# Performance work log

Measured on AMD Instinct MI355X. Metric: run time of the kernel, lower is better.

## Reference

```python
import jax, jax.numpy as jnp
import numpy as np
import math

B, T, DIM = 2, 2048, 4096
N_HEADS, N_KV_HEADS = 32, 8
HEAD_DIM = DIM // N_HEADS          # 128
N_REP = N_HEADS // N_KV_HEADS      # 4
ROPE_THETA = 500000.0
NEG_INF = -1e9


def setup_inputs() -> dict:
    key = jax.random.key(0)
    ks = jax.random.split(key, 5)
    x = jax.random.normal(ks[0], (B, T, DIM), dtype=jnp.float32)
    # rotary angles: theta_j = pos * base^(-2j/d), shape [T, HEAD_DIM//2]
    inv_freq = 1.0 / (ROPE_THETA ** (jnp.arange(0, HEAD_DIM, 2, dtype=jnp.float32) / HEAD_DIM))
    freqs = jnp.arange(T, dtype=jnp.float32)[:, None] * inv_freq[None, :]
    # causal additive mask [T, T]
    mask = jnp.where(jnp.tril(jnp.ones((T, T), dtype=bool)), 0.0, NEG_INF).astype(jnp.float32)
    s = 0.02
    wq = jax.random.normal(ks[1], (DIM, N_HEADS * HEAD_DIM), dtype=jnp.float32) * s
    wk = jax.random.normal(ks[2], (DIM, N_KV_HEADS * HEAD_DIM), dtype=jnp.float32) * s
    wv = jax.random.normal(ks[3], (DIM, N_KV_HEADS * HEAD_DIM), dtype=jnp.float32) * s
    wo = jax.random.normal(ks[4], (N_HEADS * HEAD_DIM, DIM), dtype=jnp.float32) * s
    return {"x": x, "freqs": freqs, "mask": mask, "wq": wq, "wk": wk, "wv": wv, "wo": wo, "start_pos": 0}


def _apply_rope(x, cos, sin):
    # x: [B, T, H, D]; cos/sin: [T, D//2]; adjacent pairs rotated (view-as-complex)
    xr = x[..., 0::2]
    xi = x[..., 1::2]
    c = cos[None, :, None, :]
    s = sin[None, :, None, :]
    out_r = xr * c - xi * s
    out_i = xr * s + xi * c
    return jnp.stack([out_r, out_i], axis=-1).reshape(x.shape)


def reference(x, freqs, mask, wq, wk, wv, wo, start_pos):
    Bx, Tx, C = x.shape
    xq = (x @ wq).reshape(Bx, Tx, N_HEADS, HEAD_DIM)
    xk = (x @ wk).reshape(Bx, Tx, N_KV_HEADS, HEAD_DIM)
    xv = (x @ wv).reshape(Bx, Tx, N_KV_HEADS, HEAD_DIM)
    cos, sin = jnp.cos(freqs), jnp.sin(freqs)
    xq = _apply_rope(xq, cos, sin)
    xk = _apply_rope(xk, cos, sin)
    # repeat_kv for GQA: [B, T, Hkv, D] -> [B, T, Hkv*n_rep, D]
    xk = jnp.repeat(xk, N_REP, axis=2)
    xv = jnp.repeat(xv, N_REP, axis=2)
    q = xq.transpose(0, 2, 1, 3)  # [B, H, T, D]
    k = xk.transpose(0, 2, 1, 3)
    v = xv.transpose(0, 2, 1, 3)
    scores = jnp.einsum("bhtd,bhsd->bhts", q, k) / math.sqrt(HEAD_DIM)
    scores = scores + mask[None, None, :, :]
    probs = jax.nn.softmax(scores.astype(jnp.float32), axis=-1).astype(q.dtype)
    out = jnp.einsum("bhts,bhsd->bhtd", probs, v)
    out = out.transpose(0, 2, 1, 3).reshape(Bx, Tx, -1)
    return out @ wo
```

## Files before the change

kernel.cpp:

```cpp
#include <hip/hip_runtime.h>
#include <cstdint>
#include <cstddef>

typedef float  f32x4  __attribute__((ext_vector_type(4)));
typedef short  bf16x8 __attribute__((ext_vector_type(8)));
typedef unsigned short u16;
typedef u16    u16x8  __attribute__((ext_vector_type(8)));
typedef unsigned int u32;

#define T_SEQ 2048
#define N_HEADS 32
#define N_KVH 8
#define HD 128
#define QSCALE 0.12751743648963412f

__device__ __forceinline__ u16 f2bf(float f){
  union { float f; unsigned u; } v; v.f = f;
  unsigned u = v.u;
  u += 0x7fffu + ((u >> 16) & 1u);
  return (u16)(u >> 16);
}

__device__ __forceinline__ u32 cvt_pk_bf16(float a, float b){
  u32 r;
  asm volatile("v_cvt_pk_bf16_f32 %0, %1, %2" : "=v"(r) : "v"(a), "v"(b));
  return r;
}

__device__ __forceinline__ void gll16(const void* g, void* l){
  __builtin_amdgcn_global_load_lds((const __attribute__((address_space(1))) void*)g,
                                   (__attribute__((address_space(3))) void*)l, 16, 0, 0);
}

__device__ __forceinline__ u32 lds_addr(const void* p){
  return (u32)(size_t)(__attribute__((address_space(3))) const void*)p;
}

__global__ void mk_tables(const float* __restrict__ f, float* __restrict__ c, float* __restrict__ s,
                          float* __restrict__ ct, float* __restrict__ st){
  int i = blockIdx.x*256 + threadIdx.x;
  float v = f[i];
  float cv = cosf(v), sv = sinf(v);
  c[i] = cv;
  s[i] = sv;
  int t = i >> 6, d = i & 63;
  ct[d*T_SEQ + t] = cv;
  st[d*T_SEQ + t] = sv;
}

__global__ void cvt_bf16(const float* __restrict__ in, u16* __restrict__ out){
  size_t i = (size_t)blockIdx.x*256 + threadIdx.x;
  const float4* p = (const float4*)(in + i*8);
  float4 a = p[0], b = p[1];
  u16x8 o;
  o[0]=f2bf(a.x); o[1]=f2bf(a.y); o[2]=f2bf(a.z); o[3]=f2bf(a.w);
  o[4]=f2bf(b.x); o[5]=f2bf(b.y); o[6]=f2bf(b.z); o[7]=f2bf(b.w);
  *(u16x8*)(out + i*8) = o;
}

__global__ void wtrans(const float* __restrict__ W, u16* __restrict__ Wt, int K, int N){
  __shared__ float t[32][33];
  int tx = threadIdx.x, ty = threadIdx.y;
  int nb = blockIdx.x*32, kb = blockIdx.y*32;
#pragma unroll
  for (int j=0;j<4;j++) t[ty+8*j][tx] = W[(size_t)(kb+ty+8*j)*N + nb + tx];
  __syncthreads();
#pragma unroll
  for (int j=0;j<4;j++) Wt[(size_t)(nb+ty+8*j)*K + kb + tx] = f2bf(t[tx][ty+8*j]);
}

template<int BN>
__global__ __launch_bounds__(512, 2) void gemm256(
    const u16* __restrict__ A, const u16* __restrict__ Bt,
    float* __restrict__ C, int N, int K)
{
  constexpr int NGB = BN/64;
  constexpr int NF  = BN/64;
  __shared__ u16 Ab[2][16384];
  __shared__ u16 Bb[2][BN*64];
  const int tid = threadIdx.x;
  const int w = tid >> 6, lane = tid & 63;
  const int lo = lane & 15, hi = lane >> 4;

  const int nbx = N / BN;
  const int cpx = (int)gridDim.x >> 3;
  const int swzb = ((int)blockIdx.x & 7)*cpx + ((int)blockIdx.x >> 3);
  const int bx = swzb % nbx, by = swzb / nbx;
  const int m0 = by << 8, n0 = bx * BN;
  const int wm = w >> 2, wn = w & 3;

  const int rA = tid >> 3;
  const int chg = (tid & 7) ^ (rA & 7);
  const size_t srcoff = (size_t)rA * K + chg*8;
  const u16* Ag = A  + (size_t)m0*K + srcoff;
  const u16* Bg = Bt + (size_t)n0*K + srcoff;
  const int dstc = (w*64)*8;

  f32x4 acc[8][NF];
#pragma unroll
  for (int i=0;i<8;i++)
#pragma unroll
    for (int j=0;j<NF;j++) acc[i][j] = (f32x4){0.f,0.f,0.f,0.f};

  const int NT = K >> 6;
#pragma unroll
  for (int j=0;j<4;j++)   gll16(Ag + (size_t)j*64*K, &Ab[0][j*4096 + dstc]);
#pragma unroll
  for (int j=0;j<NGB;j++) gll16(Bg + (size_t)j*64*K, &Bb[0][j*4096 + dstc]);

  const int sw = lo & 7;
#pragma unroll 1
  for (int t=0; t<NT; ++t){
    const int cur = t & 1;
    if (t > 0){
      asm volatile("s_waitcnt lgkmcnt(0)" ::: "memory");
      __builtin_amdgcn_s_barrier();
    }
    if (t + 1 < NT){
      const int kt = (t+1) << 6;
      const int nxt = cur ^ 1;
#pragma unroll
      for (int j=0;j<4;j++)   gll16(Ag + (size_t)j*64*K + kt, &Ab[nxt][j*4096 + dstc]);
#pragma unroll
      for (int j=0;j<NGB;j++) gll16(Bg + (size_t)j*64*K + kt, &Bb[nxt][j*4096 + dstc]);
      if constexpr (BN == 256){
        asm volatile("s_waitcnt vmcnt(8)" ::: "memory");
      } else {
        asm volatile("s_waitcnt vmcnt(6)" ::: "memory");
      }
    } else {
      asm volatile("s_waitcnt vmcnt(0)" ::: "memory");
    }
    __builtin_amdgcn_s_barrier();
    __builtin_amdgcn_sched_barrier(0);

    const u16* Ac = &Ab[cur][0] + (wm*128)*64;
    const u16* Bc = &Bb[cur][0] + (wn*(BN/4))*64;
    bf16x8 a[4], b[NF];
#pragma unroll
    for (int ks=0; ks<2; ks++){
      const int ch = ((ks*4 + hi) ^ sw) << 3;
#pragma unroll
      for (int g=0; g<NF; g++) b[g] = *(const bf16x8*)(Bc + (g*16 + lo)*64 + ch);
#pragma unroll
      for (int mh=0; mh<2; mh++){
#pragma unroll
        for (int f=0; f<4; f++) a[f] = *(const bf16x8*)(Ac + (mh*64 + f*16 + lo)*64 + ch);
        __builtin_amdgcn_s_setprio(1);
#pragma unroll
        for (int f=0; f<4; f++)
#pragma unroll
          for (int g=0; g<NF; g++)
            acc[mh*4+f][g] = __builtin_amdgcn_mfma_f32_16x16x32_bf16(a[f], b[g], acc[mh*4+f][g], 0, 0, 0);
        __builtin_amdgcn_s_setprio(0);
      }
    }
  }

#pragma unroll
  for (int mh=0; mh<2; mh++)
#pragma unroll
    for (int f=0; f<4; f++)
#pragma unroll
      for (int g=0; g<NF; g++)
#pragma unroll
        for (int r=0; r<4; r++)
          C[(size_t)(m0 + wm*128 + mh*64 + f*16 + hi*4 + r)*N + n0 + wn*(BN/4) + g*16 + lo] = acc[mh*4+f][g][r];
}

#define RDA(BK, RGS, MH) { _Pragma("unroll") for (int f=0; f<4; f++) \
    asm volatile("ds_read_b128 %0, %1 offset:" RGS : "=v"(BK[f]) : "v"(aAddr[MH][f])); }
#define RDB(BK, RGS) { _Pragma("unroll") for (int g=0; g<4; g++) \
    asm volatile("ds_read_b128 %0, %1 offset:" RGS : "=v"(BK[g]) : "v"(bAddr[g])); }
#define STGA8(RG, KO) { gll16(Ag + offs0 + (KO), AL + (RG) + wofs); gll16(Ag + offs1 + (KO), AL + (RG) + 4096 + wofs); }
#define STGB8(RG, KO) { gll16(Bg + offs0 + (KO), BL + (RG) + wofs); gll16(Bg + offs1 + (KO), BL + (RG) + 4096 + wofs); }
#define MFMAB(AB, BB, MH) { _Pragma("unroll") for (int f=0; f<4; f++) _Pragma("unroll") for (int g=0; g<4; g++) \
    acc[(MH)*4+f][g] = __builtin_amdgcn_mfma_f32_16x16x32_bf16(AB[f], BB[g], acc[(MH)*4+f][g], 0, 0, 0); }
#define PH_HEAD() { __builtin_amdgcn_sched_barrier(0); __builtin_amdgcn_s_barrier(); \
    asm volatile("s_waitcnt lgkmcnt(0)" ::: "memory"); __builtin_amdgcn_sched_barrier(0); __builtin_amdgcn_s_setprio(1); }
#define PH_TAIL() { __builtin_amdgcn_s_setprio(0); __builtin_amdgcn_s_barrier(); }

__global__ __launch_bounds__(512, 2) void gemm8p(
    const u16* __restrict__ A, const u16* __restrict__ Bt,
    float* __restrict__ C, int N, int K)
{
  __shared__ u16 AL[32768];
  __shared__ u16 BL[32768];
  const int tid = threadIdx.x;
  const int w = tid >> 6, lane = tid & 63;
  const int lo = lane & 15, hi = lane >> 4;

  const int nbx = N >> 8;
  const int cpx = (int)gridDim.x >> 3;
  const int swzb = ((int)blockIdx.x & 7)*cpx + ((int)blockIdx.x >> 3);
  const int bx = swzb % nbx, by = swzb / nbx;
  const int m0 = by << 8, n0 = bx << 8;
  const int wm = w >> 2, wn = w & 3;

  u32 aAddr[2][4], bAddr[4];
#pragma unroll
  for (int mh=0; mh<2; mh++)
#pragma unroll
    for (int f=0; f<4; f++){
      int row = wm*128 + mh*64 + f*16 + lo;
      int p = row >> 1;
      aAddr[mh][f] = lds_addr(AL) + (u32)((p*8 + (((row&1)*4 + hi) ^ (p&7)))*16);
    }
#pragma unroll
  for (int g=0; g<4; g++){
    int row = wn*64 + g*16 + lo;
    int p = row >> 1;
    bAddr[g] = lds_addr(BL) + (u32)((p*8 + (((row&1)*4 + hi) ^ (p&7)))*16);
  }

  int offs0, offs1;
  {
    int n = tid;
    int p = n>>3, e = (n&7) ^ (p&7);
    offs0 = (p*2 + (e>>2))*K + (e&3)*8;
    n = 512 + tid;
    p = n>>3; e = (n&7) ^ (p&7);
    offs1 = (p*2 + (e>>2))*K + (e&3)*8;
  }
  const u16* Ag = A  + (size_t)m0*K;
  const u16* Bg = Bt + (size_t)n0*K;
  const int wofs = w*512;

  f32x4 acc[8][4];
#pragma unroll
  for (int i=0;i<8;i++)
#pragma unroll
    for (int j=0;j<4;j++) acc[i][j] = (f32x4){0.f,0.f,0.f,0.f};

  const int NT = K >> 6;
  bf16x8 aA[4], aB[4], bA[4], bB[4];

  STGA8(0, 0)       STGB8(0, 0)
  STGA8(8192, 32)   STGB8(8192, 32)
  STGA8(16384, 64)  STGB8(16384, 64)
  asm volatile("s_waitcnt vmcnt(8)" ::: "memory");
  __builtin_amdgcn_s_barrier();
  RDA(aA, "0", 0) RDB(bA, "0")

#pragma unroll 1
  for (int u = 0; u < NT-2; u += 2){
    const int ku = u*64;
    STGA8(24576, ku+96)
    PH_HEAD() RDA(aB, "0", 1) MFMAB(aA, bA, 0) PH_TAIL()
    STGB8(24576, ku+96)
    asm volatile("s_waitcnt vmcnt(8)" ::: "memory");
    PH_HEAD() RDA(aA, "16384", 0) RDB(bB, "16384") MFMAB(aB, bA, 1) PH_TAIL()
    STGA8(0, ku+128)
    PH_HEAD() RDA(aB, "16384", 1) MFMAB(aA, bB, 0) PH_TAIL()
    STGB8(0, ku+128)
    asm volatile("s_waitcnt vmcnt(8)" ::: "memory");
    PH_HEAD() RDA(aA, "32768", 0) RDB(bA, "32768") MFMAB(aB, bB, 1) PH_TAIL()
    STGA8(8192, ku+160)
    PH_HEAD() RDA(aB, "32768", 1) MFMAB(aA, bA, 0) PH_TAIL()
    STGB8(8192, ku+160)
    asm volatile("s_waitcnt vmcnt(8)" ::: "memory");
    PH_HEAD() RDA(aA, "49152", 0) RDB(bB, "49152") MFMAB(aB, bA, 1) PH_TAIL()
    STGA8(16384, ku+192)
    PH_HEAD() RDA(aB, "49152", 1) MFMAB(aA, bB, 0) PH_TAIL()
    STGB8(16384, ku+192)
    asm volatile("s_waitcnt vmcnt(8)" ::: "memory");
    PH_HEAD() RDA(aA, "0", 0) RDB(bA, "0") MFMAB(aB, bB, 1) PH_TAIL()
  }

  {
    const int ku = (NT-2)*64;
    STGA8(24576, ku+96)
    PH_HEAD() RDA(aB, "0", 1) MFMAB(aA, bA, 0) PH_TAIL()
    STGB8(24576, ku+96)
    asm volatile("s_waitcnt vmcnt(8)" ::: "memory");
    PH_HEAD() RDA(aA, "16384", 0) RDB(bB, "16384") MFMAB(aB, bA, 1) PH_TAIL()
    PH_HEAD() RDA(aB, "16384", 1) MFMAB(aA, bB, 0) PH_TAIL()
    asm volatile("s_waitcnt vmcnt(4)" ::: "memory");
    PH_HEAD() RDA(aA, "32768", 0) RDB(bA, "32768") MFMAB(aB, bB, 1) PH_TAIL()
    PH_HEAD() RDA(aB, "32768", 1) MFMAB(aA, bA, 0) PH_TAIL()
    asm volatile("s_waitcnt vmcnt(0)" ::: "memory");
    PH_HEAD() RDA(aA, "49152", 0) RDB(bB, "49152") MFMAB(aB, bA, 1) PH_TAIL()
    PH_HEAD() RDA(aB, "49152", 1) MFMAB(aA, bB, 0) PH_TAIL()
    PH_HEAD() MFMAB(aB, bB, 1) PH_TAIL()
  }

#pragma unroll
  for (int mh=0; mh<2; mh++)
#pragma unroll
    for (int f=0; f<4; f++)
#pragma unroll
      for (int g=0; g<4; g++)
#pragma unroll
        for (int r=0; r<4; r++)
          C[(size_t)(m0 + wm*128 + mh*64 + f*16 + hi*4 + r)*N + n0 + wn*64 + g*16 + lo] = acc[mh*4+f][g][r];
}

__global__ void rope_k(const float* __restrict__ kvf, const float* __restrict__ c,
                       const float* __restrict__ s, u16* __restrict__ kb){
  const int row = blockIdx.x;
  const int b = row >> 11, t = row & (T_SEQ-1);
  const float* ib = kvf + (size_t)row*2048;
#pragma unroll
  for (int k=0;k<2;k++){
    int p = threadIdx.x + k*256;
    int kvh = p >> 6, i = p & 63;
    float cv = c[t*64+i], sv = s[t*64+i];
    float2 v = *(const float2*)(ib + 2*p);
    float vr = v.x*cv - v.y*sv;
    float vi = v.x*sv + v.y*cv;
    u16* o = kb + ((size_t)(b*N_KVH+kvh)*T_SEQ + t)*HD + 2*i;
    ushort2 ov; ov.x = f2bf(vr); ov.y = f2bf(vi);
    *(ushort2*)o = ov;
  }
}

__global__ void vtrans(const float* __restrict__ kvf, u16* __restrict__ vt){
  __shared__ float tl[32][33];
  int tx = threadIdx.x, ty = threadIdx.y;
  int t0 = blockIdx.x*32, d0 = blockIdx.y*32, bh = blockIdx.z;
  int b = bh >> 3, kvh = bh & 7;
#pragma unroll
  for (int j=0;j<4;j++)
    tl[ty+8*j][tx] = kvf[(size_t)(b*T_SEQ + t0+ty+8*j)*2048 + 1024 + kvh*HD + d0 + tx];
  __syncthreads();
#pragma unroll
  for (int j=0;j<4;j++)
    vt[((size_t)bh*HD + d0+ty+8*j)*T_SEQ + t0 + tx] = f2bf(tl[tx][ty+8*j]);
}

#define KVB 64
__global__ __launch_bounds__(512) void attn_kernel(
    const float* __restrict__ qf, const float* __restrict__ costT, const float* __restrict__ sintT,
    const u16* __restrict__ kb, const u16* __restrict__ vt, u16* __restrict__ attn)
{
  __shared__ u16 KV[2][2][8192];

  const int tid = threadIdx.x;
  const int lane = tid & 63, wid = tid >> 6;
  const int lo = lane & 15, hi = lane >> 4;
  const bool lowhi = (hi < 2);
  const int bp0 = lo + 32*(hi & 1);
  const int bp1 = bp0 + 16;
  const int h = blockIdx.y, b = blockIdx.z;
  const int kvh = h >> 2;
  const int qt = b ? (int)blockIdx.x : 7 - (int)blockIdx.x;
  const int q0 = qt*256 + wid*32;
  const int ntiles = (qt+1)*4;

  int koff[2], voff[2];
#pragma unroll
  for (int p=0;p<2;p++){
    int s = p*512 + tid;
    int kr = s >> 4, kch = (s & 15) ^ (kr & 7);
    koff[p] = kr*HD + kch*8;
    int vd = s >> 3, vch = (s & 7) ^ (vd & 7);
    voff[p] = vd*T_SEQ + vch*8;
  }
  const u16* Kg = kb + (size_t)(b*N_KVH + kvh)*T_SEQ*HD;
  const u16* Vg = vt + (size_t)(b*N_KVH + kvh)*HD*T_SEQ;

  bf16x8 qfr[2][4];
#pragma unroll
  for (int mb=0;mb<2;mb++){
    const int t = q0 + mb*16 + lo;
    const float* qrow = qf + (size_t)(b*T_SEQ + t)*4096 + h*HD;
#pragma unroll
    for (int kc=0;kc<4;kc++){
      f32x4 v0 = *(const f32x4*)(qrow + kc*32 + hi*8);
      f32x4 v1 = *(const f32x4*)(qrow + kc*32 + hi*8 + 4);
      union { u32 w[4]; bf16x8 v; } pk;
#pragma unroll
      for (int j=0;j<4;j++){
        int i = kc*16 + hi*4 + j;
        float cv = costT[i*T_SEQ + t], sv = sintT[i*T_SEQ + t];
        float xr = (j<2) ? v0[2*j]   : v1[2*(j-2)];
        float xi = (j<2) ? v0[2*j+1] : v1[2*(j-2)+1];
        float vr = (xr*cv - xi*sv)*QSCALE;
        float vi = (xr*sv + xi*cv)*QSCALE;
        pk.w[j] = ((u32)f2bf(vi) << 16) | (u32)f2bf(vr);
      }
      qfr[mb][kc] = pk.v;
    }
  }

  f32x4 acc[2][8];
#pragma unroll
  for (int mb=0;mb<2;mb++)
#pragma unroll
    for (int nd=0;nd<8;nd++) acc[mb][nd] = (f32x4){0.f,0.f,0.f,0.f};
  float m_[2] = {-3.0e38f, -3.0e38f};
  float l_[2] = {0.f, 0.f};

#pragma unroll
  for (int p=0;p<2;p++){
    gll16(Kg + koff[p], (u16*)&KV[0][0][0] + (p*512 + wid*64)*8);
    gll16(Vg + voff[p], (u16*)&KV[0][1][0] + (p*512 + wid*64)*8);
  }

#pragma unroll 1
  for (int st=0; st<ntiles; ++st){
    const int cur = st & 1;
    const int sb = st*KVB;
    if (st > 0){
      asm volatile("s_waitcnt lgkmcnt(0)" ::: "memory");
      __builtin_amdgcn_s_barrier();
    }
    if (st + 1 < ntiles){
      const int nxt = cur ^ 1;
      const int nb2 = (st+1)*KVB;
#pragma unroll
      for (int p=0;p<2;p++){
        gll16(Kg + nb2*HD + koff[p], (u16*)&KV[nxt][0][0] + (p*512 + wid*64)*8);
        gll16(Vg + nb2    + voff[p], (u16*)&KV[nxt][1][0] + (p*512 + wid*64)*8);
      }
      asm volatile("s_waitcnt vmcnt(4)" ::: "memory");
    } else {
      asm volatile("s_waitcnt vmcnt(0)" ::: "memory");
    }
    __builtin_amdgcn_s_barrier();

    const bool live = (sb <= q0 + 31);
    if (live){
      f32x4 sc[2][4];
#pragma unroll
      for (int mb=0;mb<2;mb++)
#pragma unroll
        for (int ns=0;ns<4;ns++) sc[mb][ns] = (f32x4){0.f,0.f,0.f,0.f};
      __builtin_amdgcn_s_setprio(1);
#pragma unroll
      for (int ns=0;ns<4;ns++){
        const int row = ns*16 + lo;
        const u16* klp = (const u16*)&KV[cur][0][0] + row*HD;
        const int sw = row & 7;
        bf16x8 kf[4];
#pragma unroll
        for (int kc=0;kc<4;kc++) kf[kc] = *(const bf16x8*)(klp + (((kc*4+hi)^sw)<<3));
#pragma unroll
        for (int kc=0;kc<4;kc++){
          sc[0][ns] = __builtin_amdgcn_mfma_f32_16x16x32_bf16(kf[kc], qfr[0][kc], sc[0][ns], 0, 0, 0);
          sc[1][ns] = __builtin_amdgcn_mfma_f32_16x16x32_bf16(kf[kc], qfr[1][kc], sc[1][ns], 0, 0, 0);
        }
      }
      __builtin_amdgcn_s_setprio(0);

      if (sb + 63 > q0){
#pragma unroll
        for (int mb=0;mb<2;mb++){
          const int qg = q0 + mb*16 + lo;
#pragma unroll
          for (int ns=0;ns<4;ns++)
#pragma unroll
            for (int r=0;r<4;r++){
              int sg = sb + ns*16 + hi*4 + r;
              if (sg > qg) sc[mb][ns][r] = -3.0e38f;
            }
        }
      }

      bf16x8 pa[2][2];
#pragma unroll
      for (int mb=0;mb<2;mb++){
        float mx = fmaxf(fmaxf(fmaxf(sc[mb][0][0],sc[mb][0][1]),fmaxf(sc[mb][0][2],sc[mb][0][3])),
                   fmaxf(fmaxf(fmaxf(sc[mb][1][0],sc[mb][1][1]),fmaxf(sc[mb][1][2],sc[mb][1][3])),
                         fmaxf(fmaxf(sc[mb][2][0],sc[mb][2][1]),
                               fmaxf(fmaxf(sc[mb][2][2],sc[mb][2][3]),
                                     fmaxf(fmaxf(sc[mb][3][0],sc[mb][3][1]),fmaxf(sc[mb][3][2],sc[mb][3][3]))))));
        mx = fmaxf(mx, __shfl_xor(mx, 16));
        mx = fmaxf(mx, __shfl_xor(mx, 32));
        if (__any(mx > m_[mb] + 8.f)){
          float mn = fmaxf(m_[mb], mx);
          float scal = exp2f(m_[mb] - mn);
          m_[mb] = mn;
          l_[mb] *= scal;
          float srow[4];
#pragma unroll
          for (int r=0;r<4;r++) srow[r] = __shfl(scal, hi*4+r);
#pragma unroll
          for (int nd=0;nd<8;nd++)
#pragma unroll
            for (int r=0;r<4;r++) acc[mb][nd][r] *= srow[r];
        }
        float rs = 0.f;
#pragma unroll
        for (int ns=0;ns<4;ns++)
#pragma unroll
          for (int r=0;r<4;r++){
            sc[mb][ns][r] = exp2f(sc[mb][ns][r] - m_[mb]);
            rs += sc[mb][ns][r];
          }
        rs += __shfl_xor(rs, 16);
        rs += __shfl_xor(rs, 32);
        l_[mb] += rs;

#pragma unroll
        for (int k2=0;k2<2;k2++){
          u32 P0 = cvt_pk_bf16(sc[mb][2*k2][0],   sc[mb][2*k2][1]);
          u32 P1 = cvt_pk_bf16(sc[mb][2*k2][2],   sc[mb][2*k2][3]);
          u32 Q0 = cvt_pk_bf16(sc[mb][2*k2+1][0], sc[mb][2*k2+1][1]);
          u32 Q1 = cvt_pk_bf16(sc[mb][2*k2+1][2], sc[mb][2*k2+1][3]);
          u32 pA0 = (u32)__shfl((int)P0, bp0);
          u32 pA1 = (u32)__shfl((int)P1, bp0);
          u32 pA2 = (u32)__shfl((int)P0, bp1);
          u32 pA3 = (u32)__shfl((int)P1, bp1);
          u32 qA0 = (u32)__shfl((int)Q0, bp0);
          u32 qA1 = (u32)__shfl((int)Q1, bp0);
          u32 qA2 = (u32)__shfl((int)Q0, bp1);
          u32 qA3 = (u32)__shfl((int)Q1, bp1);
          union { u32 w[4]; bf16x8 v; } pk;
          pk.w[0] = lowhi ? pA0 : qA0;
          pk.w[1] = lowhi ? pA1 : qA1;
          pk.w[2] = lowhi ? pA2 : qA2;
          pk.w[3] = lowhi ? pA3 : qA3;
          pa[mb][k2] = pk.v;
        }
      }

      __builtin_amdgcn_s_setprio(1);
#pragma unroll
      for (int nd=0;nd<8;nd++){
        const int d = nd*16 + lo;
        const u16* vlp = (const u16*)&KV[cur][1][0] + d*64;
        const int sw = d & 7;
        bf16x8 vf[2];
#pragma unroll
        for (int k2=0;k2<2;k2++) vf[k2] = *(const bf16x8*)(vlp + (((k2*4+hi)^sw)<<3));
#pragma unroll
        for (int k2=0;k2<2;k2++){
          acc[0][nd] = __builtin_amdgcn_mfma_f32_16x16x32_bf16(pa[0][k2], vf[k2], acc[0][nd], 0, 0, 0);
          acc[1][nd] = __builtin_amdgcn_mfma_f32_16x16x32_bf16(pa[1][k2], vf[k2], acc[1][nd], 0, 0, 0);
        }
      }
      __builtin_amdgcn_s_setprio(0);
    }
  }

#pragma unroll
  for (int mb=0;mb<2;mb++){
    float inv = 1.f / l_[mb];
    float invr[4];
#pragma unroll
    for (int r=0;r<4;r++) invr[r] = __shfl(inv, hi*4+r);
    u16* ob = attn + (size_t)(b*T_SEQ + q0 + mb*16 + hi*4)*4096 + h*HD;
#pragma unroll
    for (int nd=0;nd<8;nd++)
#pragma unroll
      for (int r=0;r<4;r++)
        ob[(size_t)r*4096 + nd*16 + lo] = f2bf(acc[mb][nd][r]*invr[r]);
  }
}

extern "C" void kernel_launch(void* const* d_in, const int* in_sizes, int n_in,
                              void* d_out, int out_size, void* d_ws, size_t ws_size,
                              hipStream_t stream)
{
  (void)in_sizes; (void)n_in; (void)out_size; (void)ws_size;
  const float* x     = (const float*)d_in[0];
  const float* freqs = (const float*)d_in[1];
  const float* wq    = (const float*)d_in[3];
  const float* wk    = (const float*)d_in[4];
  const float* wv    = (const float*)d_in[5];
  const float* wo    = (const float*)d_in[6];

  char* ws = (char*)d_ws;
  float* cost  = (float*)(ws + 0);
  float* sint  = (float*)(ws + 524288);
  u16* xb   = (u16*)(ws + 1048576);
  u16* wqt  = (u16*)(ws + 34603008);
  u16* wkt  = (u16*)(ws + 68157440);
  u16* wvt  = (u16*)(ws + 76546048);
  float* kvf = (float*)(ws + 84934656);
  u16* kbuf = (u16*)(ws + 118489088);
  u16* vbuf = (u16*)(ws + 126877696);
  u16* attnb = xb;
  u16* wot   = wqt;
  float* costT = (float*)(ws + 68157440);
  float* sintT = (float*)(ws + 68681728);

  float* qf = (float*)d_out;

  dim3 tb(32, 8);

  cvt_bf16<<<8192, 256, 0, stream>>>(x, xb);
  wtrans<<<dim3(128,128), tb, 0, stream>>>(wq, wqt, 4096, 4096);
  wtrans<<<dim3(32,128),  tb, 0, stream>>>(wk, wkt, 4096, 1024);
  wtrans<<<dim3(32,128),  tb, 0, stream>>>(wv, wvt, 4096, 1024);

  gemm8p<<<dim3(256), 512, 0, stream>>>(xb, wqt, qf, 4096, 4096);

  gemm256<128><<<dim3(256), 512, 0, stream>>>(xb, wkt, kvf, 2048, 4096);

  mk_tables<<<512, 256, 0, stream>>>(freqs, cost, sint, costT, sintT);

  rope_k<<<4096, 256, 0, stream>>>(kvf, cost, sint, kbuf);
  vtrans<<<dim3(64,4,16), tb, 0, stream>>>(kvf, vbuf);

  attn_kernel<<<dim3(8,32,2), 512, 0, stream>>>(qf, costT, sintT, kbuf, vbuf, attnb);

  wtrans<<<dim3(128,128), tb, 0, stream>>>(wo, wot, 4096, 4096);
  gemm8p<<<dim3(256), 512, 0, stream>>>(attnb, wot, (float*)d_out, 4096, 4096);
}
```

Before: 553.4 us.

## Merge half-phases in gemm8p pipeline into full-tile phases with double-buffered fragments

Restructures the 8-wave GEMM main loop from eight half-tile phases per iteration (each issuing one A half or B load and 16 MFMAs) into four full phases that each read all A and B fragments for the next k-slice and issue 32 MFMAs. A and B global-to-LDS loads are grouped into a single STG4 per phase. This halves the number of barrier/waitcnt phases per k-step, cutting synchronisation overhead, but raises register pressure because two full fragment sets (aX/bX, aY/bY) are held, and it changes the vmcnt wait placement.

```diff
diff --git a/kernel.cpp b/kernel.cpp
--- a/kernel.cpp
+++ b/kernel.cpp
@@ -168,14 +168,19 @@
           C[(size_t)(m0 + wm*128 + mh*64 + f*16 + hi*4 + r)*N + n0 + wn*(BN/4) + g*16 + lo] = acc[mh*4+f][g][r];
 }
 
-#define RDA(BK, RGS, MH) { _Pragma("unroll") for (int f=0; f<4; f++) \
-    asm volatile("ds_read_b128 %0, %1 offset:" RGS : "=v"(BK[f]) : "v"(aAddr[MH][f])); }
-#define RDB(BK, RGS) { _Pragma("unroll") for (int g=0; g<4; g++) \
-    asm volatile("ds_read_b128 %0, %1 offset:" RGS : "=v"(BK[g]) : "v"(bAddr[g])); }
-#define STGA8(RG, KO) { gll16(Ag + offs0 + (KO), AL + (RG) + wofs); gll16(Ag + offs1 + (KO), AL + (RG) + 4096 + wofs); }
-#define STGB8(RG, KO) { gll16(Bg + offs0 + (KO), BL + (RG) + wofs); gll16(Bg + offs1 + (KO), BL + (RG) + 4096 + wofs); }
-#define MFMAB(AB, BB, MH) { _Pragma("unroll") for (int f=0; f<4; f++) _Pragma("unroll") for (int g=0; g<4; g++) \
-    acc[(MH)*4+f][g] = __builtin_amdgcn_mfma_f32_16x16x32_bf16(AB[f], BB[g], acc[(MH)*4+f][g], 0, 0, 0); }
+#define RDP(AA, BB, RGS) { \
+  _Pragma("unroll") for (int mh=0; mh<2; mh++) \
+  _Pragma("unroll") for (int f=0; f<4; f++) \
+    asm volatile("ds_read_b128 %0, %1 offset:" RGS : "=v"(AA[mh][f]) : "v"(aAddr[mh][f])); \
+  _Pragma("unroll") for (int g=0; g<4; g++) \
+    asm volatile("ds_read_b128 %0, %1 offset:" RGS : "=v"(BB[g]) : "v"(bAddr[g])); }
+#define STG4(RG, KO) { gll16(Ag + offs0 + (KO), AL + (RG) + wofs); gll16(Ag + offs1 + (KO), AL + (RG) + 4096 + wofs); \
+                       gll16(Bg + offs0 + (KO), BL + (RG) + wofs); gll16(Bg + offs1 + (KO), BL + (RG) + 4096 + wofs); }
+#define MFMAP(AA, BB) { \
+  _Pragma("unroll") for (int mh=0; mh<2; mh++) \
+  _Pragma("unroll") for (int f=0; f<4; f++) \
+  _Pragma("unroll") for (int g=0; g<4; g++) \
+    acc[mh*4+f][g] = __builtin_amdgcn_mfma_f32_16x16x32_bf16(AA[mh][f], BB[g], acc[mh*4+f][g], 0, 0, 0); }
 #define PH_HEAD() { __builtin_amdgcn_sched_barrier(0); __builtin_amdgcn_s_barrier(); \
     asm volatile("s_waitcnt lgkmcnt(0)" ::: "memory"); __builtin_amdgcn_sched_barrier(0); __builtin_amdgcn_s_setprio(1); }
 #define PH_TAIL() { __builtin_amdgcn_s_setprio(0); __builtin_amdgcn_s_barrier(); }
@@ -233,55 +238,42 @@
     for (int j=0;j<4;j++) acc[i][j] = (f32x4){0.f,0.f,0.f,0.f};
 
   const int NT = K >> 6;
-  bf16x8 aA[4], aB[4], bA[4], bB[4];
-
-  STGA8(0, 0)       STGB8(0, 0)
-  STGA8(8192, 32)   STGB8(8192, 32)
-  STGA8(16384, 64)  STGB8(16384, 64)
-  asm volatile("s_waitcnt vmcnt(8)" ::: "memory");
+  bf16x8 aX[2][4], bX[4], aY[2][4], bY[4];
+
+  STG4(0, 0)
+  STG4(8192, 32)
+  STG4(16384, 64)
+  asm volatile("s_waitcnt vmcnt(4)" ::: "memory");
   __builtin_amdgcn_s_barrier();
-  RDA(aA, "0", 0) RDB(bA, "0")
+  RDP(aX, bX, "0")
 
 #pragma unroll 1
   for (int u = 0; u < NT-2; u += 2){
     const int ku = u*64;
-    STGA8(24576, ku+96)
-    PH_HEAD() RDA(aB, "0", 1) MFMAB(aA, bA, 0) PH_TAIL()
-    STGB8(24576, ku+96)
+    STG4(24576, ku+96)
     asm volatile("s_waitcnt vmcnt(8)" ::: "memory");
-    PH_HEAD() RDA(aA, "16384", 0) RDB(bB, "16384") MFMAB(aB, bA, 1) PH_TAIL()
-    STGA8(0, ku+128)
-    PH_HEAD() RDA(aB, "16384", 1) MFMAB(aA, bB, 0) PH_TAIL()
-    STGB8(0, ku+128)
+    PH_HEAD() RDP(aY, bY, "16384") MFMAP(aX, bX) PH_TAIL()
+    STG4(0, ku+128)
     asm volatile("s_waitcnt vmcnt(8)" ::: "memory");
-    PH_HEAD() RDA(aA, "32768", 0) RDB(bA, "32768") MFMAB(aB, bB, 1) PH_TAIL()
-    STGA8(8192, ku+160)
-    PH_HEAD() RDA(aB, "32768", 1) MFMAB(aA, bA, 0) PH_TAIL()
-    STGB8(8192, ku+160)
+    PH_HEAD() RDP(aX, bX, "32768") MFMAP(aY, bY) PH_TAIL()
+    STG4(8192, ku+160)
     asm volatile("s_waitcnt vmcnt(8)" ::: "memory");
-    PH_HEAD() RDA(aA, "49152", 0) RDB(bB, "49152") MFMAB(aB, bA, 1) PH_TAIL()
-    STGA8(16384, ku+192)
-    PH_HEAD() RDA(aB, "49152", 1) MFMAB(aA, bB, 0) PH_TAIL()
-    STGB8(16384, ku+192)
+    PH_HEAD() RDP(aY, bY, "49152") MFMAP(aX, bX) PH_TAIL()
+    STG4(16384, ku+192)
     asm volatile("s_waitcnt vmcnt(8)" ::: "memory");
-    PH_HEAD() RDA(aA, "0", 0) RDB(bA, "0") MFMAB(aB, bB, 1) PH_TAIL()
+    PH_HEAD() RDP(aX, bX, "0") MFMAP(aY, bY) PH_TAIL()
   }
 
   {
     const int ku = (NT-2)*64;
-    STGA8(24576, ku+96)
-    PH_HEAD() RDA(aB, "0", 1) MFMAB(aA, bA, 0) PH_TAIL()
-    STGB8(24576, ku+96)
+    STG4(24576, ku+96)
     asm volatile("s_waitcnt vmcnt(8)" ::: "memory");
-    PH_HEAD() RDA(aA, "16384", 0) RDB(bB, "16384") MFMAB(aB, bA, 1) PH_TAIL()
-    PH_HEAD() RDA(aB, "16384", 1) MFMAB(aA, bB, 0) PH_TAIL()
+    PH_HEAD() RDP(aY, bY, "16384") MFMAP(aX, bX) PH_TAIL()
     asm volatile("s_waitcnt vmcnt(4)" ::: "memory");
-    PH_HEAD() RDA(aA, "32768", 0) RDB(bA, "32768") MFMAB(aB, bB, 1) PH_TAIL()
-    PH_HEAD() RDA(aB, "32768", 1) MFMAB(aA, bA, 0) PH_TAIL()
+    PH_HEAD() RDP(aX, bX, "32768") MFMAP(aY, bY) PH_TAIL()
     asm volatile("s_waitcnt vmcnt(0)" ::: "memory");
-    PH_HEAD() RDA(aA, "49152", 0) RDB(bB, "49152") MFMAB(aB, bA, 1) PH_TAIL()
-    PH_HEAD() RDA(aB, "49152", 1) MFMAB(aA, bB, 0) PH_TAIL()
-    PH_HEAD() MFMAB(aB, bB, 1) PH_TAIL()
+    PH_HEAD() RDP(aY, bY, "49152") MFMAP(aX, bX) PH_TAIL()
+    PH_HEAD() MFMAP(aY, bY) PH_TAIL()
   }
 
 #pragma unroll
```

After: 561.9 us. Within noise of the previous version (+1.5%).
